# Optimization experiments

Measured on AMD Instinct MI355X. Metric: run time of the kernel, lower is better.

## Reference

```python
import jax, jax.numpy as jnp
import numpy as np

NEG_SLOPE = 0.2  # PyG GATConv default


def add_self_loops(edge_index, num_nodes):
    loops = jnp.arange(num_nodes, dtype=edge_index.dtype)
    return jnp.concatenate([edge_index, jnp.stack([loops, loops])], axis=1)


def gat_conv(x, edge_index, W, att_src, att_dst, bias, heads, out_ch, concat):
    # x: [N, F_in]; edge_index: [2, E] with row0=src(j), row1=dst(i)
    N = x.shape[0]
    xl = (x @ W).reshape(N, heads, out_ch)              # [N, H, C]
    src, dst = edge_index[0], edge_index[1]
    a_src = jnp.einsum('nhc,hc->nh', xl, att_src)        # [N, H]
    a_dst = jnp.einsum('nhc,hc->nh', xl, att_dst)        # [N, H]
    alpha = jax.nn.leaky_relu(a_src[src] + a_dst[dst], NEG_SLOPE)  # [E, H]
    # segment softmax over incoming edges of each dst node
    m = jax.ops.segment_max(alpha, dst, num_segments=N)  # [N, H]
    e = jnp.exp(alpha - m[dst])
    denom = jax.ops.segment_sum(e, dst, num_segments=N)
    coef = e / (denom[dst] + 1e-16)                      # [E, H]
    msg = xl[src] * coef[..., None]                      # [E, H, C]
    out = jax.ops.segment_sum(msg, dst, num_segments=N)  # [N, H, C]
    out = out.reshape(N, heads * out_ch) if concat else out.mean(axis=1)
    return out + bias


def setup_inputs() -> dict:
    key = jax.random.key(0)
    ks = jax.random.split(key, 12)
    N, E = 50000, 800000
    nfeat, nhid, nheads, nclass = 512, 8, 8, 16
    hid = nhid * nheads  # 64
    s1 = 1.0 / np.sqrt(nfeat)
    s2 = 1.0 / np.sqrt(hid)
    return {
        'x': jax.random.normal(ks[0], (N, nfeat), jnp.float32),
        'edge_index': jax.random.randint(ks[1], (2, E), 0, N, jnp.int64 if jax.config.jax_enable_x64 else jnp.int32),
        'W1': jax.random.uniform(ks[2], (nfeat, hid), jnp.float32, -s1, s1),
        'att_src1': jax.random.uniform(ks[3], (nheads, nhid), jnp.float32, -s2, s2),
        'att_dst1': jax.random.uniform(ks[4], (nheads, nhid), jnp.float32, -s2, s2),
        'bias1': jnp.zeros((hid,), jnp.float32),
        'W2': jax.random.uniform(ks[5], (hid, nclass), jnp.float32, -s2, s2),
        'att_src2': jax.random.uniform(ks[6], (1, nclass), jnp.float32, -0.25, 0.25),
        'att_dst2': jax.random.uniform(ks[7], (1, nclass), jnp.float32, -0.25, 0.25),
        'bias2': jnp.zeros((nclass,), jnp.float32),
    }


def reference(x, edge_index, W1, att_src1, att_dst1, bias1, W2, att_src2, att_dst2, bias2):
    N = x.shape[0]
    ei = add_self_loops(edge_index, N)
    # dropout layers are identity at inference
    h = gat_conv(x, ei, W1, att_src1, att_dst1, bias1, heads=8, out_ch=8, concat=True)
    o = gat_conv(h, ei, W2, att_src2, att_dst2, bias2, heads=1, out_ch=16, concat=True)
    o = jax.nn.elu(o)
    return jax.nn.log_softmax(o, axis=1)
```

## Files before the change

### kernel.cpp

```cpp
#include <hip/hip_runtime.h>
#include <math.h>

#define NEG_SLOPE 0.2f

typedef short short8 __attribute__((ext_vector_type(8)));
typedef float floatx4 __attribute__((ext_vector_type(4)));

static __device__ __forceinline__ float bf2f(unsigned short u) {
  return __uint_as_float(((unsigned int)u) << 16);
}
static __device__ __forceinline__ unsigned short f2bf(float f) {
  unsigned int u = __float_as_uint(f);
  u = (u + 0x7fffu + ((u >> 16) & 1u)) >> 16;
  return (unsigned short)u;
}
static __device__ __forceinline__ unsigned int pack2(float a, float b) {
  return (unsigned int)f2bf(a) | ((unsigned int)f2bf(b) << 16);
}

__global__ void conv_w1(const float* __restrict__ W1, unsigned short* __restrict__ W1t) {
  int i = blockIdx.x * 256 + threadIdx.x;
  int k = i >> 6, c = i & 63;
  W1t[c * 512 + k] = f2bf(W1[i]);
}

__global__ __launch_bounds__(256) void gemm1_mfma(const float* __restrict__ A,
                                                  const unsigned short* __restrict__ W1t,
                                                  const float* __restrict__ att_src,
                                                  const float* __restrict__ att_dst,
                                                  unsigned short* __restrict__ xlb,
                                                  float* __restrict__ a_src,
                                                  float* __restrict__ a_dst, int M) {
  __shared__ unsigned short As[64 * 72];
  __shared__ unsigned short Bs[64 * 72];
  int tid = threadIdx.x;
  int w = tid >> 6, lane = tid & 63;
  int q = lane >> 4, cl = lane & 15;
  int row0 = blockIdx.x << 6;
  floatx4 acc[4] = {};

  int sr = tid >> 2;
  int skq = (tid & 3) << 4;
  int arow = row0 + sr;
  const float* Aptr = A + (size_t)arow * 512 + skq;
  const unsigned short* Bptr = W1t + sr * 512 + skq;
  unsigned short* AsW = As + sr * 72 + skq;
  unsigned short* BsW = Bs + sr * 72 + skq;

  for (int k0 = 0; k0 < 512; k0 += 64) {
    float4 f0 = make_float4(0.f, 0.f, 0.f, 0.f), f1 = f0, f2 = f0, f3 = f0;
    if (arow < M) {
      f0 = *(const float4*)(Aptr + k0);
      f1 = *(const float4*)(Aptr + k0 + 4);
      f2 = *(const float4*)(Aptr + k0 + 8);
      f3 = *(const float4*)(Aptr + k0 + 12);
    }
    uint4 b0 = *(const uint4*)(Bptr + k0);
    uint4 b1 = *(const uint4*)(Bptr + k0 + 8);
    __syncthreads();
    uint4 a0, a1;
    a0.x = pack2(f0.x, f0.y); a0.y = pack2(f0.z, f0.w);
    a0.z = pack2(f1.x, f1.y); a0.w = pack2(f1.z, f1.w);
    a1.x = pack2(f2.x, f2.y); a1.y = pack2(f2.z, f2.w);
    a1.z = pack2(f3.x, f3.y); a1.w = pack2(f3.z, f3.w);
    *(uint4*)(AsW) = a0;
    *(uint4*)(AsW + 8) = a1;
    *(uint4*)(BsW) = b0;
    *(uint4*)(BsW + 8) = b1;
    __syncthreads();
#pragma unroll
    for (int kk = 0; kk < 2; ++kk) {
      short8 af = *(const short8*)(As + (w * 16 + cl) * 72 + kk * 32 + q * 8);
#pragma unroll
      for (int t = 0; t < 4; ++t) {
        short8 bf = *(const short8*)(Bs + (t * 16 + cl) * 72 + kk * 32 + q * 8);
        acc[t] = __builtin_amdgcn_mfma_f32_16x16x32_bf16(af, bf, acc[t], 0, 0, 0);
      }
    }
  }

  float asv[4], adv[4];
#pragma unroll
  for (int t = 0; t < 4; ++t) {
    asv[t] = att_src[t * 16 + cl];
    adv[t] = att_dst[t * 16 + cl];
  }
#pragma unroll
  for (int reg = 0; reg < 4; ++reg) {
    int r = row0 + w * 16 + q * 4 + reg;
    bool ok = r < M;
#pragma unroll
    for (int t = 0; t < 4; ++t) {
      float v = acc[t][reg];
      if (ok) xlb[(size_t)r * 64 + t * 16 + cl] = f2bf(v);
      float ps = v * asv[t];
      float pd = v * adv[t];
      ps += __shfl_xor(ps, 1); pd += __shfl_xor(pd, 1);
      ps += __shfl_xor(ps, 2); pd += __shfl_xor(pd, 2);
      ps += __shfl_xor(ps, 4); pd += __shfl_xor(pd, 4);
      if (ok && (cl & 7) == 0) {
        int h = t * 2 + (cl >> 3);
        a_src[r * 8 + h] = ps;
        a_dst[r * 8 + h] = pd;
      }
    }
  }
}

__global__ void deg_init(int* __restrict__ deg, int N) {
  int n = blockIdx.x * blockDim.x + threadIdx.x;
  if (n < N) deg[n] = 1;
}

__global__ __launch_bounds__(256) void deg_hist_sliced(const int* __restrict__ ei,
                                                       int* __restrict__ deg,
                                                       int E, int N, int ipc) {
  int slice = blockIdx.x & 7;
  int chunk = blockIdx.x >> 3;
  int lo = (int)(((long long)slice * N) >> 3);
  int hi = (int)(((long long)(slice + 1) * N) >> 3);
  int beg = chunk * ipc;
  int end = min(beg + ipc, E);
  for (int i = beg + threadIdx.x; i < end; i += 256) {
    int d = ei[E + i];
    if (d >= lo && d < hi) atomicAdd(&deg[d], 1);
  }
}

__global__ __launch_bounds__(256) void partial_sums(const int* __restrict__ deg,
                                                    int* __restrict__ partials, int N) {
  __shared__ int ws[4];
  int base = blockIdx.x * 512;
  int tid = threadIdx.x;
  int i0 = base + tid * 2;
  int s = 0;
  if (i0 < N) s += deg[i0];
  if (i0 + 1 < N) s += deg[i0 + 1];
#pragma unroll
  for (int off = 32; off >= 1; off >>= 1) s += __shfl_xor(s, off, 64);
  if ((tid & 63) == 0) ws[tid >> 6] = s;
  __syncthreads();
  if (tid == 0) partials[blockIdx.x] = ws[0] + ws[1] + ws[2] + ws[3];
}

__global__ __launch_bounds__(256) void scan_partials(const int* __restrict__ partials,
                                                     int* __restrict__ blockoff,
                                                     int* __restrict__ rowptr, int nb, int N) {
  __shared__ int sums[256];
  int tid = threadIdx.x;
  int chunk = (nb + 255) >> 8;
  int start = tid * chunk, end = min(start + chunk, nb);
  int s = 0;
  for (int i = start; i < end; ++i) s += partials[i];
  sums[tid] = s;
  __syncthreads();
  for (int off = 1; off < 256; off <<= 1) {
    int t = (tid >= off) ? sums[tid - off] : 0;
    __syncthreads();
    sums[tid] += t;
    __syncthreads();
  }
  int run = (tid == 0) ? 0 : sums[tid - 1];
  for (int i = start; i < end; ++i) {
    blockoff[i] = run;
    run += partials[i];
  }
  if (tid == 255) rowptr[N] = sums[255];
}

__global__ __launch_bounds__(256) void scan_blocks(const int* __restrict__ deg,
                                                   const int* __restrict__ blockoff,
                                                   int* __restrict__ rowptr,
                                                   int* __restrict__ cursor, int N) {
  __shared__ int wavesum[4];
  int base = blockIdx.x * 512;
  int tid = threadIdx.x;
  int lane = tid & 63, wv = tid >> 6;
  int i0 = base + tid * 2;
  int d0 = (i0 < N) ? deg[i0] : 0;
  int d1 = (i0 + 1 < N) ? deg[i0 + 1] : 0;
  int s = d0 + d1;
  int v = s;
#pragma unroll
  for (int off = 1; off < 64; off <<= 1) {
    int t = __shfl_up(v, off, 64);
    if (lane >= off) v += t;
  }
  if (lane == 63) wavesum[wv] = v;
  __syncthreads();
  int woff = 0;
  for (int w = 0; w < wv; ++w) woff += wavesum[w];
  int excl = v - s + woff + blockoff[blockIdx.x];
  if (i0 < N) { rowptr[i0] = excl; cursor[i0] = excl; }
  if (i0 + 1 < N) { rowptr[i0 + 1] = excl + d0; cursor[i0 + 1] = excl + d0; }
}

__global__ __launch_bounds__(256) void scatter_sliced(const int* __restrict__ ei,
                                                      int* __restrict__ cursor,
                                                      int* __restrict__ srcs,
                                                      int E, int N, int ipc) {
  int slice = blockIdx.x & 7;
  int chunk = blockIdx.x >> 3;
  int lo = (int)(((long long)slice * N) >> 3);
  int hi = (int)(((long long)(slice + 1) * N) >> 3);
  int total = E + N;
  int beg = chunk * ipc;
  int end = min(beg + ipc, total);
  for (int i = beg + threadIdx.x; i < end; i += 256) {
    int d = (i < E) ? ei[E + i] : (i - E);
    if (d >= lo && d < hi) {
      int s = (i < E) ? ei[i] : d;
      int pos = atomicAdd(&cursor[d], 1);
      srcs[pos] = s;
    }
  }
}

__global__ __launch_bounds__(256) void agg1_csr(const int* __restrict__ rowptr,
                                                const int* __restrict__ srcs,
                                                const float* __restrict__ a_src,
                                                const float* __restrict__ a_dst,
                                                const unsigned short* __restrict__ xlb,
                                                float* __restrict__ agg1, int N) {
  int wave = (blockIdx.x * blockDim.x + threadIdx.x) >> 6;
  int lane = threadIdx.x & 63;
  if (wave >= N) return;
  int h = lane >> 3;
  int beg = rowptr[wave], end = rowptr[wave + 1];
  float ad = a_dst[wave * 8 + h];
  float den = 0.f, acc = 0.f;
  int p = beg;
  for (; p + 4 <= end; p += 4) {
    int s0 = srcs[p], s1 = srcs[p + 1], s2 = srcs[p + 2], s3 = srcs[p + 3];
    float a0 = a_src[s0 * 8 + h], a1 = a_src[s1 * 8 + h];
    float a2 = a_src[s2 * 8 + h], a3 = a_src[s3 * 8 + h];
    float x0 = bf2f(xlb[(size_t)s0 * 64 + lane]);
    float x1 = bf2f(xlb[(size_t)s1 * 64 + lane]);
    float x2 = bf2f(xlb[(size_t)s2 * 64 + lane]);
    float x3 = bf2f(xlb[(size_t)s3 * 64 + lane]);
    a0 += ad; a1 += ad; a2 += ad; a3 += ad;
    a0 = a0 >= 0.f ? a0 : NEG_SLOPE * a0;
    a1 = a1 >= 0.f ? a1 : NEG_SLOPE * a1;
    a2 = a2 >= 0.f ? a2 : NEG_SLOPE * a2;
    a3 = a3 >= 0.f ? a3 : NEG_SLOPE * a3;
    float w0 = __expf(a0), w1 = __expf(a1), w2 = __expf(a2), w3 = __expf(a3);
    den += (w0 + w1) + (w2 + w3);
    acc += w0 * x0 + w1 * x1 + w2 * x2 + w3 * x3;
  }
  for (; p < end; ++p) {
    int s = srcs[p];
    float a = a_src[s * 8 + h] + ad;
    a = a >= 0.f ? a : NEG_SLOPE * a;
    float w = __expf(a);
    den += w;
    acc += w * bf2f(xlb[(size_t)s * 64 + lane]);
  }
  agg1[(size_t)wave * 64 + lane] = acc / (den + 1e-16f);
}

__global__ __launch_bounds__(256) void gemm2_prep(const float* __restrict__ agg1,
                                                  const float* __restrict__ bias1,
                                                  const float* __restrict__ W2,
                                                  const float* __restrict__ att_src2,
                                                  const float* __restrict__ att_dst2,
                                                  float* __restrict__ xl2,
                                                  float* __restrict__ a_src2,
                                                  float* __restrict__ a_dst2, int N) {
  __shared__ float hs[16 * 68];
  int tid = threadIdx.x;
  int n0 = blockIdx.x << 4;
  {
    int node = tid >> 4;
    int off = (tid & 15) << 2;
    int nn = n0 + node;
    float4 v = make_float4(0.f, 0.f, 0.f, 0.f);
    if (nn < N) {
      v = *(const float4*)(agg1 + (size_t)nn * 64 + off);
      float4 b = *(const float4*)(bias1 + off);
      v.x += b.x; v.y += b.y; v.z += b.z; v.w += b.w;
    }
    *(float4*)(hs + node * 68 + off) = v;
  }
  __syncthreads();
  int t = tid >> 4, c = tid & 15;
  int n = n0 + t;
  if (n >= N) return;
  float sum = 0.f;
#pragma unroll
  for (int k = 0; k < 64; ++k) sum += hs[t * 68 + k] * W2[k * 16 + c];
  xl2[(size_t)n * 16 + c] = sum;
  float ps = sum * att_src2[c];
  float pd = sum * att_dst2[c];
#pragma unroll
  for (int w = 8; w >= 1; w >>= 1) {
    ps += __shfl_xor(ps, w, 16);
    pd += __shfl_xor(pd, w, 16);
  }
  if (c == 0) {
    a_src2[n] = ps;
    a_dst2[n] = pd;
  }
}

__global__ __launch_bounds__(256) void agg2_fin(const int* __restrict__ rowptr,
                                                const int* __restrict__ srcs,
                                                const float* __restrict__ a_src2,
                                                const float* __restrict__ a_dst2,
                                                const float* __restrict__ xl2,
                                                const float* __restrict__ bias2,
                                                float* __restrict__ out, int N) {
  int t = blockIdx.x * blockDim.x + threadIdx.x;
  int node = t >> 4;
  int c = t & 15;
  if (node >= N) return;
  int beg = rowptr[node], end = rowptr[node + 1];
  float ad = a_dst2[node];
  float den = 0.f, acc = 0.f;
  int p = beg;
  for (; p + 4 <= end; p += 4) {
    int s0 = srcs[p], s1 = srcs[p + 1], s2 = srcs[p + 2], s3 = srcs[p + 3];
    float a0 = a_src2[s0], a1 = a_src2[s1], a2 = a_src2[s2], a3 = a_src2[s3];
    float x0 = xl2[(size_t)s0 * 16 + c], x1 = xl2[(size_t)s1 * 16 + c];
    float x2 = xl2[(size_t)s2 * 16 + c], x3 = xl2[(size_t)s3 * 16 + c];
    a0 += ad; a1 += ad; a2 += ad; a3 += ad;
    a0 = a0 >= 0.f ? a0 : NEG_SLOPE * a0;
    a1 = a1 >= 0.f ? a1 : NEG_SLOPE * a1;
    a2 = a2 >= 0.f ? a2 : NEG_SLOPE * a2;
    a3 = a3 >= 0.f ? a3 : NEG_SLOPE * a3;
    float w0 = __expf(a0), w1 = __expf(a1), w2 = __expf(a2), w3 = __expf(a3);
    den += (w0 + w1) + (w2 + w3);
    acc += w0 * x0 + w1 * x1 + w2 * x2 + w3 * x3;
  }
  for (; p < end; ++p) {
    int s = srcs[p];
    float a = a_src2[s] + ad;
    a = a >= 0.f ? a : NEG_SLOPE * a;
    float w = __expf(a);
    den += w;
    acc += w * xl2[(size_t)s * 16 + c];
  }
  float o = acc / (den + 1e-16f) + bias2[c];
  o = o > 0.f ? o : expm1f(o);
  float mx = o;
#pragma unroll
  for (int w = 8; w >= 1; w >>= 1) mx = fmaxf(mx, __shfl_xor(mx, w, 16));
  float e = __expf(o - mx);
  float ssum = e;
#pragma unroll
  for (int w = 8; w >= 1; w >>= 1) ssum += __shfl_xor(ssum, w, 16);
  out[(size_t)node * 16 + c] = o - mx - logf(ssum);
}

extern "C" void kernel_launch(void* const* d_in, const int* in_sizes, int n_in,
                              void* d_out, int out_size, void* d_ws, size_t ws_size,
                              hipStream_t stream) {
  const float* x        = (const float*)d_in[0];
  const int*   ei       = (const int*)d_in[1];
  const float* W1       = (const float*)d_in[2];
  const float* att_src1 = (const float*)d_in[3];
  const float* att_dst1 = (const float*)d_in[4];
  const float* bias1    = (const float*)d_in[5];
  const float* W2       = (const float*)d_in[6];
  const float* att_src2 = (const float*)d_in[7];
  const float* att_dst2 = (const float*)d_in[8];
  const float* bias2    = (const float*)d_in[9];
  float* out = (float*)d_out;

  int N = in_sizes[0] / 512;
  int E = in_sizes[1] / 2;
  int nb = (N + 511) / 512;

  char* ws = (char*)d_ws;
  unsigned short* xlb = (unsigned short*)ws;        ws += (size_t)N * 64 * 2;
  unsigned short* W1t = (unsigned short*)ws;        ws += (size_t)512 * 64 * 2;
  float* a_src1 = (float*)ws;                       ws += (size_t)N * 8 * 4;
  float* a_dst1 = (float*)ws;                       ws += (size_t)N * 8 * 4;
  float* agg1   = (float*)ws;                       ws += (size_t)N * 64 * 4;
  float* xl2    = (float*)ws;                       ws += (size_t)N * 16 * 4;
  float* a_src2 = (float*)ws;                       ws += (size_t)N * 4;
  float* a_dst2 = (float*)ws;                       ws += (size_t)N * 4;
  int* deg      = (int*)ws;                         ws += (size_t)N * 4;
  int* rowptr   = (int*)ws;                         ws += (size_t)(N + 1) * 4;
  int* cursor   = (int*)ws;                         ws += (size_t)N * 4;
  int* srcs     = (int*)ws;                         ws += (size_t)(E + N) * 4;
  int* partials = (int*)ws;                         ws += (size_t)nb * 4;
  int* blockoff = (int*)ws;                         ws += (size_t)nb * 4;

  const int NCHUNK = 256;
  int ipc_h = (E + NCHUNK - 1) / NCHUNK;
  int ipc_s = (E + N + NCHUNK - 1) / NCHUNK;
  deg_init<<<(N + 255) / 256, 256, 0, stream>>>(deg, N);
  deg_hist_sliced<<<NCHUNK * 8, 256, 0, stream>>>(ei, deg, E, N, ipc_h);
  partial_sums<<<nb, 256, 0, stream>>>(deg, partials, N);
  scan_partials<<<1, 256, 0, stream>>>(partials, blockoff, rowptr, nb, N);
  scan_blocks<<<nb, 256, 0, stream>>>(deg, blockoff, rowptr, cursor, N);
  scatter_sliced<<<NCHUNK * 8, 256, 0, stream>>>(ei, cursor, srcs, E, N, ipc_s);

  conv_w1<<<128, 256, 0, stream>>>(W1, W1t);
  gemm1_mfma<<<(N + 63) / 64, 256, 0, stream>>>(x, W1t, att_src1, att_dst1,
                                                xlb, a_src1, a_dst1, N);
  agg1_csr<<<((size_t)N * 64 + 255) / 256, 256, 0, stream>>>(rowptr, srcs, a_src1, a_dst1,
                                                             xlb, agg1, N);

  gemm2_prep<<<(N + 15) / 16, 256, 0, stream>>>(agg1, bias1, W2, att_src2, att_dst2,
                                                xl2, a_src2, a_dst2, N);
  agg2_fin<<<((size_t)N * 16 + 255) / 256, 256, 0, stream>>>(rowptr, srcs, a_src2, a_dst2,
                                                             xl2, bias2, out, N);
}
```

Baseline: 333.6 us.

## Fuse init kernels, prefetch GEMM1 tiles, split agg1 edges across half-waves

Merges the W1 transpose and degree-initialisation kernels into one launch to save a kernel launch. In gemm1, global loads for the next K tile are issued before the MFMA work on the current tile, so load latency overlaps compute at the cost of extra registers. agg1 now has each half-wave handle alternate edges with two bf16 features per lane, then combines the halves with a cross-half shuffle. This gives fewer, wider gathers per edge pair.

```diff
diff --git a/kernel.cpp b/kernel.cpp
--- a/kernel.cpp
+++ b/kernel.cpp
@@ -18,10 +18,17 @@
   return (unsigned int)f2bf(a) | ((unsigned int)f2bf(b) << 16);
 }
 
-__global__ void conv_w1(const float* __restrict__ W1, unsigned short* __restrict__ W1t) {
-  int i = blockIdx.x * 256 + threadIdx.x;
-  int k = i >> 6, c = i & 63;
-  W1t[c * 512 + k] = f2bf(W1[i]);
+__global__ void init_misc(const float* __restrict__ W1, unsigned short* __restrict__ W1t,
+                          int* __restrict__ deg, int N) {
+  int b = blockIdx.x;
+  if (b < 128) {
+    int i = b * 256 + threadIdx.x;
+    int k = i >> 6, c = i & 63;
+    W1t[c * 512 + k] = f2bf(W1[i]);
+  } else {
+    int n = (b - 128) * 256 + threadIdx.x;
+    if (n < N) deg[n] = 1;
+  }
 }
 
 __global__ __launch_bounds__(256) void gemm1_mfma(const float* __restrict__ A,
@@ -42,32 +49,47 @@
   int sr = tid >> 2;
   int skq = (tid & 3) << 4;
   int arow = row0 + sr;
+  bool okA = arow < M;
   const float* Aptr = A + (size_t)arow * 512 + skq;
   const unsigned short* Bptr = W1t + sr * 512 + skq;
   unsigned short* AsW = As + sr * 72 + skq;
   unsigned short* BsW = Bs + sr * 72 + skq;
 
+  float4 ca0 = make_float4(0.f, 0.f, 0.f, 0.f), ca1 = ca0, ca2 = ca0, ca3 = ca0;
+  uint4 cb0, cb1;
+  if (okA) {
+    ca0 = *(const float4*)(Aptr);
+    ca1 = *(const float4*)(Aptr + 4);
+    ca2 = *(const float4*)(Aptr + 8);
+    ca3 = *(const float4*)(Aptr + 12);
+  }
+  cb0 = *(const uint4*)(Bptr);
+  cb1 = *(const uint4*)(Bptr + 8);
+
+#pragma unroll
   for (int k0 = 0; k0 < 512; k0 += 64) {
-    float4 f0 = make_float4(0.f, 0.f, 0.f, 0.f), f1 = f0, f2 = f0, f3 = f0;
-    if (arow < M) {
-      f0 = *(const float4*)(Aptr + k0);
-      f1 = *(const float4*)(Aptr + k0 + 4);
-      f2 = *(const float4*)(Aptr + k0 + 8);
-      f3 = *(const float4*)(Aptr + k0 + 12);
-    }
-    uint4 b0 = *(const uint4*)(Bptr + k0);
-    uint4 b1 = *(const uint4*)(Bptr + k0 + 8);
     __syncthreads();
     uint4 a0, a1;
-    a0.x = pack2(f0.x, f0.y); a0.y = pack2(f0.z, f0.w);
-    a0.z = pack2(f1.x, f1.y); a0.w = pack2(f1.z, f1.w);
-    a1.x = pack2(f2.x, f2.y); a1.y = pack2(f2.z, f2.w);
-    a1.z = pack2(f3.x, f3.y); a1.w = pack2(f3.z, f3.w);
+    a0.x = pack2(ca0.x, ca0.y); a0.y = pack2(ca0.z, ca0.w);
+    a0.z = pack2(ca1.x, ca1.y); a0.w = pack2(ca1.z, ca1.w);
+    a1.x = pack2(ca2.x, ca2.y); a1.y = pack2(ca2.z, ca2.w);
+    a1.z = pack2(ca3.x, ca3.y); a1.w = pack2(ca3.z, ca3.w);
     *(uint4*)(AsW) = a0;
     *(uint4*)(AsW + 8) = a1;
-    *(uint4*)(BsW) = b0;
-    *(uint4*)(BsW + 8) = b1;
+    *(uint4*)(BsW) = cb0;
+    *(uint4*)(BsW + 8) = cb1;
     __syncthreads();
+    if (k0 < 448) {
+      ca0 = make_float4(0.f, 0.f, 0.f, 0.f); ca1 = ca0; ca2 = ca0; ca3 = ca0;
+      if (okA) {
+        ca0 = *(const float4*)(Aptr + k0 + 64);
+        ca1 = *(const float4*)(Aptr + k0 + 68);
+        ca2 = *(const float4*)(Aptr + k0 + 72);
+        ca3 = *(const float4*)(Aptr + k0 + 76);
+      }
+      cb0 = *(const uint4*)(Bptr + k0 + 64);
+      cb1 = *(const uint4*)(Bptr + k0 + 72);
+    }
 #pragma unroll
     for (int kk = 0; kk < 2; ++kk) {
       short8 af = *(const short8*)(As + (w * 16 + cl) * 72 + kk * 32 + q * 8);
@@ -105,11 +127,6 @@
       }
     }
   }
-}
-
-__global__ void deg_init(int* __restrict__ deg, int N) {
-  int n = blockIdx.x * blockDim.x + threadIdx.x;
-  if (n < N) deg[n] = 1;
 }
 
 __global__ __launch_bounds__(256) void deg_hist_sliced(const int* __restrict__ ei,
@@ -225,37 +242,47 @@
   int wave = (blockIdx.x * blockDim.x + threadIdx.x) >> 6;
   int lane = threadIdx.x & 63;
   if (wave >= N) return;
-  int h = lane >> 3;
+  int half = lane >> 5;
+  int j = lane & 31;
+  int h = j >> 2;
   int beg = rowptr[wave], end = rowptr[wave + 1];
   float ad = a_dst[wave * 8 + h];
-  float den = 0.f, acc = 0.f;
+  float den = 0.f, acc0 = 0.f, acc1 = 0.f;
   int p = beg;
   for (; p + 4 <= end; p += 4) {
-    int s0 = srcs[p], s1 = srcs[p + 1], s2 = srcs[p + 2], s3 = srcs[p + 3];
-    float a0 = a_src[s0 * 8 + h], a1 = a_src[s1 * 8 + h];
-    float a2 = a_src[s2 * 8 + h], a3 = a_src[s3 * 8 + h];
-    float x0 = bf2f(xlb[(size_t)s0 * 64 + lane]);
-    float x1 = bf2f(xlb[(size_t)s1 * 64 + lane]);
-    float x2 = bf2f(xlb[(size_t)s2 * 64 + lane]);
-    float x3 = bf2f(xlb[(size_t)s3 * 64 + lane]);
-    a0 += ad; a1 += ad; a2 += ad; a3 += ad;
-    a0 = a0 >= 0.f ? a0 : NEG_SLOPE * a0;
-    a1 = a1 >= 0.f ? a1 : NEG_SLOPE * a1;
-    a2 = a2 >= 0.f ? a2 : NEG_SLOPE * a2;
-    a3 = a3 >= 0.f ? a3 : NEG_SLOPE * a3;
-    float w0 = __expf(a0), w1 = __expf(a1), w2 = __expf(a2), w3 = __expf(a3);
-    den += (w0 + w1) + (w2 + w3);
-    acc += w0 * x0 + w1 * x1 + w2 * x2 + w3 * x3;
-  }
-  for (; p < end; ++p) {
-    int s = srcs[p];
-    float a = a_src[s * 8 + h] + ad;
-    a = a >= 0.f ? a : NEG_SLOPE * a;
-    float w = __expf(a);
-    den += w;
-    acc += w * bf2f(xlb[(size_t)s * 64 + lane]);
-  }
-  agg1[(size_t)wave * 64 + lane] = acc / (den + 1e-16f);
+    int sA = srcs[p + half];
+    int sB = srcs[p + 2 + half];
+    float aA = a_src[sA * 8 + h] + ad;
+    float aB = a_src[sB * 8 + h] + ad;
+    ushort2 xA = *(const ushort2*)(xlb + (size_t)sA * 64 + 2 * j);
+    ushort2 xB = *(const ushort2*)(xlb + (size_t)sB * 64 + 2 * j);
+    aA = aA >= 0.f ? aA : NEG_SLOPE * aA;
+    aB = aB >= 0.f ? aB : NEG_SLOPE * aB;
+    float wA = __expf(aA), wB = __expf(aB);
+    den += wA + wB;
+    acc0 += wA * bf2f(xA.x) + wB * bf2f(xB.x);
+    acc1 += wA * bf2f(xA.y) + wB * bf2f(xB.y);
+  }
+  for (; p < end; p += 2) {
+    int idx = p + half;
+    if (idx < end) {
+      int s = srcs[idx];
+      float a = a_src[s * 8 + h] + ad;
+      ushort2 x = *(const ushort2*)(xlb + (size_t)s * 64 + 2 * j);
+      a = a >= 0.f ? a : NEG_SLOPE * a;
+      float w = __expf(a);
+      den += w;
+      acc0 += w * bf2f(x.x);
+      acc1 += w * bf2f(x.y);
+    }
+  }
+  den += __shfl_xor(den, 32);
+  acc0 += __shfl_xor(acc0, 32);
+  acc1 += __shfl_xor(acc1, 32);
+  if (half == 0) {
+    float inv = 1.f / (den + 1e-16f);
+    *(float2*)(agg1 + (size_t)wave * 64 + 2 * j) = make_float2(acc0 * inv, acc1 * inv);
+  }
 }
 
 __global__ __launch_bounds__(256) void gemm2_prep(const float* __restrict__ agg1,
@@ -386,17 +413,17 @@
   int* partials = (int*)ws;                         ws += (size_t)nb * 4;
   int* blockoff = (int*)ws;                         ws += (size_t)nb * 4;
 
+  init_misc<<<128 + (N + 255) / 256, 256, 0, stream>>>(W1, W1t, deg, N);
+
   const int NCHUNK = 256;
   int ipc_h = (E + NCHUNK - 1) / NCHUNK;
   int ipc_s = (E + N + NCHUNK - 1) / NCHUNK;
-  deg_init<<<(N + 255) / 256, 256, 0, stream>>>(deg, N);
   deg_hist_sliced<<<NCHUNK * 8, 256, 0, stream>>>(ei, deg, E, N, ipc_h);
   partial_sums<<<nb, 256, 0, stream>>>(deg, partials, N);
   scan_partials<<<1, 256, 0, stream>>>(partials, blockoff, rowptr, nb, N);
   scan_blocks<<<nb, 256, 0, stream>>>(deg, blockoff, rowptr, cursor, N);
   scatter_sliced<<<NCHUNK * 8, 256, 0, stream>>>(ei, cursor, srcs, E, N, ipc_s);
 
-  conv_w1<<<128, 256, 0, stream>>>(W1, W1t);
   gemm1_mfma<<<(N + 63) / 64, 256, 0, stream>>>(x, W1t, att_src1, att_dst1,
                                                 xlb, a_src1, a_dst1, N);
   agg1_csr<<<((size_t)N * 64 + 255) / 256, 256, 0, stream>>>(rowptr, srcs, a_src1, a_dst1,
```

Result: faster. 325.2 us (-2.5%).
